# Optimization experiments

Hardware: AMD Instinct MI355X
Metric: run time of the kernel (lower is better)

The kernel has to match this reference:

```python
import jax, jax.numpy as jnp
import numpy as np

B, H, L, N = 8, 512, 2048, 64  # batch, channels (vmapped width), seq len (l_max), state size
DT_MIN, DT_MAX = 0.01, 1.0


def setup_inputs() -> dict:
    key = jax.random.key(0)
    k1, k2, k3 = jax.random.split(key, 3)
    u = jax.random.normal(k1, (B, H, L), dtype=jnp.float32)
    # 'lin' scaling init: A_re = -0.5, A_im = pi * arange(N), per channel
    A_re = -0.5 * jnp.ones((H, N), jnp.float32)
    A_im = jnp.pi * jnp.broadcast_to(jnp.arange(N, dtype=jnp.float32), (H, N))
    C = jax.random.normal(k2, (H, N, 2), jnp.float32) * jnp.float32(0.5 ** 0.5)
    D = jnp.ones((H,), jnp.float32)
    log_step = (jax.random.uniform(k3, (H,), jnp.float32)
                * (jnp.log(DT_MAX) - jnp.log(DT_MIN)) + jnp.log(DT_MIN))
    return dict(u=u, A_re=A_re, A_im=A_im, C=C, D=D, log_step=log_step)


def reference(u, A_re, A_im, C, D, log_step):
    Lq = u.shape[-1]
    # A = clip(A_re, max=-1e-4) + i*A_im  (H, N) complex
    A = jnp.minimum(A_re, -1e-4) + 1j * A_im
    Cc = C[..., 0] + 1j * C[..., 1]                 # (H, N)
    step = jnp.exp(log_step)                        # (H,)
    dtA = step[:, None] * A                         # (H, N)
    # ZOH kernel: K[h,l] = Re( sum_n C[h,n] * (exp(dtA)-1)/A * exp(dtA)^l )
    coef = Cc * (jnp.exp(dtA) - 1.0) / A            # (H, N)
    ells = jnp.arange(Lq, dtype=jnp.float32)
    expmat = jnp.exp(dtA[:, :, None] * ells)        # (H, N, L) complex
    K = jnp.einsum('hn,hnl->hl', coef, expmat).real  # (H, L)
    # FFT causal convolution: pad to 2L (as in the original: pad u by len(K), K by len(u))
    n2 = 2 * Lq
    Ud = jnp.fft.rfft(u, n=n2, axis=-1)             # (B, H, L+1)
    Kd = jnp.fft.rfft(K, n=n2, axis=-1)             # (H, L+1)
    conv = jnp.fft.irfft(Ud * Kd[None], n=n2, axis=-1)[..., :Lq]
    return conv + D[None, :, None] * u
```

## Files before the change

kernel.cpp:

```cpp
#include <hip/hip_runtime.h>
#include <math.h>


typedef short bf16x8 __attribute__((ext_vector_type(8)));
typedef float f32x4  __attribute__((ext_vector_type(4)));

#define NCHK 32
#define USTR 68
#define ESTR 66
#define MFMA __builtin_amdgcn_mfma_f32_16x16x32_bf16

static __device__ __forceinline__ short f2bf(float x){
    unsigned u = __float_as_uint(x);
    u += 0x7FFFu + ((u >> 16) & 1u);
    return (short)(u >> 16);
}
static __device__ __forceinline__ float bf2f(short h){
    return __uint_as_float(((unsigned)(unsigned short)h) << 16);
}
static __device__ __forceinline__ void split8(const float* f, bf16x8& hi, bf16x8& lo){
    #pragma unroll
    for (int i=0;i<8;++i){
        const short hv = f2bf(f[i]);
        hi[i] = hv;
        lo[i] = f2bf(f[i] - bf2f(hv));
    }
}
static __device__ __forceinline__ void cmul(float& xr, float& xi, float yr, float yi){
    const float t = xr*yr - xi*yi;
    xi = xr*yi + xi*yr;
    xr = t;
}

__global__ void __launch_bounds__(256, 3) s4d_mfma4(
    const float* __restrict__ u_g, const float* __restrict__ A_re,
    const float* __restrict__ A_im, const float* __restrict__ Cg,
    const float* __restrict__ Dp, const float* __restrict__ log_step,
    float* __restrict__ out, int B, int H, int L)
{
    const int h    = blockIdx.x;
    const int tid  = threadIdx.x;
    const int wv   = tid >> 6;
    const int lane = tid & 63;
    const int l15  = lane & 15;
    const int oct  = lane >> 4;

    __shared__ __align__(16) float u_s[2][NCHK][USTR];
    __shared__ __align__(16) char  pool2[34816];
    __shared__ float K_s[64];

    float (*w_s)[NCHK][USTR] = (float (*)[NCHK][USTR])pool2;
    float (*S_s)[NCHK][USTR] = (float (*)[NCHK][USTR])(pool2 + 17408);
    float* Ef = (float*)pool2;

    const float dt = expf(log_step[h]);

    const float are = fminf(A_re[h*64 + lane], -1e-4f);
    const float aim = A_im[h*64 + lane];
    const float dre = dt * are, dim = dt * aim;
    float sn_, cs_;
    const float er = expf(dre);
    sincosf(dim, &sn_, &cs_);
    const float rre = er * cs_, rim = er * sn_;
    const float den = are*are + aim*aim;
    const float ir  = are/den, ii = -aim/den;
    const float c0r = Cg[(h*64+lane)*2 + 0];
    const float c0i = Cg[(h*64+lane)*2 + 1];
    const float e1r = rre - 1.0f, e1i = rim;
    const float ttr = e1r*ir - e1i*ii;
    const float tti = e1r*ii + e1i*ir;
    const float cre = c0r*ttr - c0i*tti;
    const float cim = c0r*tti + c0i*ttr;

    {
        const float* up = u_g + (size_t)h * (size_t)L;
        float4 a0 = *(const float4*)(up + tid*8);
        float4 a1 = *(const float4*)(up + tid*8 + 4);
        const int ch = (tid*8) >> 6, t0 = (tid*8) & 63;
        *(float4*)&u_s[0][ch][t0]   = a0;
        *(float4*)&u_s[0][ch][t0+4] = a1;
    }

    float rhor, rhoi;
    {
        float qre = rre, qim = rim;
        #pragma unroll
        for (int i=0;i<4;++i){ const float t2=qre*qre-qim*qim; qim=2.0f*qre*qim; qre=t2; }
        rhor = qre; rhoi = qim;
        cmul(rhor, rhoi, rhor, rhoi);
        cmul(rhor, rhoi, rhor, rhoi);
        float wre = 1.0f, wim = 0.0f;
        for (int i=0;i<wv;++i) cmul(wre, wim, qre, qim);
        float mre = cre*wre - cim*wim;
        float mim = cre*wim + cim*wre;
        #pragma unroll
        for (int jj=0;jj<16;++jj){
            const int p = wv*16 + jj;
            float red = mre;
            #pragma unroll
            for (int off=32; off; off>>=1) red += __shfl_xor(red, off);
            if (lane == 0) K_s[p] = red;
            Ef[p*ESTR + lane]      = mre;
            Ef[(65+p)*ESTR + lane] = -mim;
            cmul(mre, mim, rre, rim);
        }
        if (wv == 3){
            Ef[64*ESTR + lane]      = mre;
            Ef[(65+64)*ESTR + lane] = -mim;
        }
    }
    __syncthreads();

    bf16x8 Whre[2], Wlre[2], Whim[2], Wlim[2];
    bf16x8 Mhre[2], Mlre[2], Mhni[2], Mlni[2];
    bf16x8 Th[2],  Tl[2];
    {
        const int nw = wv*16 + l15;
        const float aw = fminf(A_re[h*64+nw], -1e-4f);
        const float bw = A_im[h*64+nw];
        const float dr = dt*aw, di = dt*bw;
        float s1, c1; const float e1 = expf(dr); sincosf(di, &s1, &c1);
        const float rwr = e1*c1, rwi = e1*s1;
        #pragma unroll
        for (int kh=0; kh<2; ++kh){
            const int elo = 63 - (kh*32 + oct*8) - 7;
            float s2, c2;
            const float e2 = expf(dr*(float)elo); sincosf(di*(float)elo, &s2, &c2);
            float vr = e2*c2, vi = e2*s2;
            float fr[8], fi[8];
            fr[7] = vr; fi[7] = vi;
            #pragma unroll
            for (int i=6;i>=0;--i){
                cmul(vr, vi, rwr, rwi);
                fr[i] = vr; fi[i] = vi;
            }
            split8(fr, Whre[kh], Wlre[kh]);
            split8(fi, Whim[kh], Wlim[kh]);
        }
        const int jp1 = wv*16 + l15 + 1;
        #pragma unroll
        for (int kh=0; kh<2; ++kh){
            const int n0 = kh*32 + oct*8;
            float fm[8];
            #pragma unroll
            for (int i=0;i<8;++i) fm[i] = Ef[jp1*ESTR + n0 + i];
            split8(fm, Mhre[kh], Mlre[kh]);
            #pragma unroll
            for (int i=0;i<8;++i) fm[i] = Ef[(65+jp1)*ESTR + n0 + i];
            split8(fm, Mhni[kh], Mlni[kh]);
            float ft[8];
            #pragma unroll
            for (int i=0;i<8;++i){
                const int d = (wv*16 + l15) - (n0 + i);
                ft[i] = (d > 0) ? K_s[d] : 0.0f;
            }
            split8(ft, Th[kh], Tl[kh]);
        }
    }
    const float DK = Dp[h] + K_s[0];
    __syncthreads();

    for (int b=0; b<B; ++b){
        const int buf = b & 1;
        const size_t obase = ((size_t)b*H + h) * (size_t)L;
        float4 p0 = {0,0,0,0}, p1 = {0,0,0,0};
        const bool pf = (b+1 < B);
        if (pf){
            const float* up = u_g + ((size_t)(b+1)*H + h) * (size_t)L;
            p0 = *(const float4*)(up + tid*8);
            p1 = *(const float4*)(up + tid*8 + 4);
        }
        bf16x8 Uh[2][2], Ul[2][2];
        #pragma unroll
        for (int ct=0; ct<2; ++ct){
            const int ch = ct*16 + l15;
            #pragma unroll
            for (int kh=0; kh<2; ++kh){
                const float4 x0 = *(const float4*)&u_s[buf][ch][kh*32 + oct*8];
                const float4 x1 = *(const float4*)&u_s[buf][ch][kh*32 + oct*8 + 4];
                const float f[8] = {x0.x,x0.y,x0.z,x0.w,x1.x,x1.y,x1.z,x1.w};
                split8(f, Uh[ct][kh], Ul[ct][kh]);
            }
        }
        #pragma unroll
        for (int ct=0; ct<2; ++ct){
            f32x4 ar = {0.f,0.f,0.f,0.f}, ai = {0.f,0.f,0.f,0.f};
            #pragma unroll
            for (int kh=0; kh<2; ++kh){
                ar = MFMA(Whre[kh], Uh[ct][kh], ar, 0,0,0);
                ar = MFMA(Whre[kh], Ul[ct][kh], ar, 0,0,0);
                ar = MFMA(Wlre[kh], Uh[ct][kh], ar, 0,0,0);
                ai = MFMA(Whim[kh], Uh[ct][kh], ai, 0,0,0);
                ai = MFMA(Whim[kh], Ul[ct][kh], ai, 0,0,0);
                ai = MFMA(Wlim[kh], Uh[ct][kh], ai, 0,0,0);
            }
            const int ch = ct*16 + l15;
            const int n0 = wv*16 + oct*4;
            *(f32x4*)&w_s[0][ch][n0] = ar;
            *(f32x4*)&w_s[1][ch][n0] = ai;
        }
        __syncthreads();
        if (wv == 0){
            float sr = 0.0f, si = 0.0f;
            #pragma unroll 4
            for (int k=0;k<NCHK;++k){
                S_s[0][k][lane] = sr; S_s[1][k][lane] = si;
                const float wr = w_s[0][k][lane];
                const float wi = w_s[1][k][lane];
                const float t2 = fmaf(rhor, sr, fmaf(-rhoi, si, wr));
                si = fmaf(rhor, si, fmaf(rhoi, sr, wi));
                sr = t2;
            }
        }
        __syncthreads();
        #pragma unroll
        for (int ct=0; ct<2; ++ct){
            const int ch = ct*16 + l15;
            bf16x8 Srh[2], Srl[2], Sih[2], Sil[2];
            #pragma unroll
            for (int kh=0; kh<2; ++kh){
                {
                    const float4 x0 = *(const float4*)&S_s[0][ch][kh*32+oct*8];
                    const float4 x1 = *(const float4*)&S_s[0][ch][kh*32+oct*8+4];
                    const float f[8] = {x0.x,x0.y,x0.z,x0.w,x1.x,x1.y,x1.z,x1.w};
                    split8(f, Srh[kh], Srl[kh]);
                }
                {
                    const float4 x0 = *(const float4*)&S_s[1][ch][kh*32+oct*8];
                    const float4 x1 = *(const float4*)&S_s[1][ch][kh*32+oct*8+4];
                    const float f[8] = {x0.x,x0.y,x0.z,x0.w,x1.x,x1.y,x1.z,x1.w};
                    split8(f, Sih[kh], Sil[kh]);
                }
            }
            f32x4 acc = {0.f,0.f,0.f,0.f};
            #pragma unroll
            for (int kh=0; kh<2; ++kh){
                acc = MFMA(Mhre[kh], Srh[kh], acc, 0,0,0);
                acc = MFMA(Mhre[kh], Srl[kh], acc, 0,0,0);
                acc = MFMA(Mlre[kh], Srh[kh], acc, 0,0,0);
                acc = MFMA(Mhni[kh], Sih[kh], acc, 0,0,0);
                acc = MFMA(Mhni[kh], Sil[kh], acc, 0,0,0);
                acc = MFMA(Mlni[kh], Sih[kh], acc, 0,0,0);
                acc = MFMA(Th[kh], Uh[ct][kh], acc, 0,0,0);
                acc = MFMA(Th[kh], Ul[ct][kh], acc, 0,0,0);
                acc = MFMA(Tl[kh], Uh[ct][kh], acc, 0,0,0);
            }
            const int j0 = wv*16 + oct*4;
            const float4 uu = *(const float4*)&u_s[buf][ch][j0];
            float4 y;
            y.x = acc[0] + DK*uu.x;
            y.y = acc[1] + DK*uu.y;
            y.z = acc[2] + DK*uu.z;
            y.w = acc[3] + DK*uu.w;
            *(float4*)(out + obase + (size_t)(ch*64 + j0)) = y;
        }
        if (pf){
            const int ch2 = (tid*8) >> 6, t0 = (tid*8) & 63;
            *(float4*)&u_s[buf^1][ch2][t0]   = p0;
            *(float4*)&u_s[buf^1][ch2][t0+4] = p1;
        }
        __syncthreads();
    }
}

extern "C" void kernel_launch(void* const* d_in, const int* in_sizes, int n_in,
                              void* d_out, int out_size, void* d_ws, size_t ws_size,
                              hipStream_t stream) {
    const float* u        = (const float*)d_in[0];
    const float* A_re     = (const float*)d_in[1];
    const float* A_im     = (const float*)d_in[2];
    const float* C        = (const float*)d_in[3];
    const float* Dp       = (const float*)d_in[4];
    const float* log_step = (const float*)d_in[5];
    float* out = (float*)d_out;

    const int H = in_sizes[4];
    const int L = 2048;
    const int B = in_sizes[0] / (H * L);
    (void)d_ws; (void)ws_size; (void)out_size; (void)n_in;

    dim3 grid(H);
    dim3 block(256);
    hipLaunchKernelGGL(s4d_mfma4, grid, block, 0, stream,
                       u, A_re, A_im, C, Dp, log_step, out, B, H, L);
}
```

Baseline: 56.46 us.

## Double block to 512 threads, split chunk tiles across wave pairs, stage output through LDS

Raises the block size from 256 to 512 threads (8 waves). Each wave now handles one 16-channel chunk tile per batch instead of two, which halves the per-wave MFMA work and register footprint. The kernel power rho = r^64 is now computed as (r^8)^8 to match the new 8-wave E-table setup. Outputs are written to LDS and then stored fully coalesced, one float4 per thread, at the cost of an extra __syncthreads per batch. The serial scan still runs on a single wave, so more waves mostly adds latency hiding and more barrier cost.

```diff
diff --git a/kernel.cpp b/kernel.cpp
--- a/kernel.cpp
+++ b/kernel.cpp
@@ -32,7 +32,7 @@
     xr = t;
 }
 
-__global__ void __launch_bounds__(256, 3) s4d_mfma4(
+__global__ void __launch_bounds__(512, 4) s4d_r8(
     const float* __restrict__ u_g, const float* __restrict__ A_re,
     const float* __restrict__ A_im, const float* __restrict__ Cg,
     const float* __restrict__ Dp, const float* __restrict__ log_step,
@@ -41,6 +41,8 @@
     const int h    = blockIdx.x;
     const int tid  = threadIdx.x;
     const int wv   = tid >> 6;
+    const int wr   = wv & 3;
+    const int wc   = wv >> 2;
     const int lane = tid & 63;
     const int l15  = lane & 15;
     const int oct  = lane >> 4;
@@ -74,28 +76,26 @@
 
     {
         const float* up = u_g + (size_t)h * (size_t)L;
-        float4 a0 = *(const float4*)(up + tid*8);
-        float4 a1 = *(const float4*)(up + tid*8 + 4);
-        const int ch = (tid*8) >> 6, t0 = (tid*8) & 63;
-        *(float4*)&u_s[0][ch][t0]   = a0;
-        *(float4*)&u_s[0][ch][t0+4] = a1;
+        const float4 a0 = *(const float4*)(up + tid*4);
+        const int ch = tid >> 4, t0 = (tid & 15) * 4;
+        *(float4*)&u_s[0][ch][t0] = a0;
     }
 
     float rhor, rhoi;
     {
-        float qre = rre, qim = rim;
-        #pragma unroll
-        for (int i=0;i<4;++i){ const float t2=qre*qre-qim*qim; qim=2.0f*qre*qim; qre=t2; }
-        rhor = qre; rhoi = qim;
-        cmul(rhor, rhoi, rhor, rhoi);
-        cmul(rhor, rhoi, rhor, rhoi);
+        float r8r = rre, r8i = rim;
+        #pragma unroll
+        for (int i=0;i<3;++i){ const float t2=r8r*r8r-r8i*r8i; r8i=2.0f*r8r*r8i; r8r=t2; }
+        rhor = r8r; rhoi = r8i;
+        #pragma unroll
+        for (int i=0;i<3;++i){ const float t2=rhor*rhor-rhoi*rhoi; rhoi=2.0f*rhor*rhoi; rhor=t2; }
         float wre = 1.0f, wim = 0.0f;
-        for (int i=0;i<wv;++i) cmul(wre, wim, qre, qim);
+        for (int i=0;i<wv;++i) cmul(wre, wim, r8r, r8i);
         float mre = cre*wre - cim*wim;
         float mim = cre*wim + cim*wre;
         #pragma unroll
-        for (int jj=0;jj<16;++jj){
-            const int p = wv*16 + jj;
+        for (int jj=0;jj<8;++jj){
+            const int p = wv*8 + jj;
             float red = mre;
             #pragma unroll
             for (int off=32; off; off>>=1) red += __shfl_xor(red, off);
@@ -104,7 +104,7 @@
             Ef[(65+p)*ESTR + lane] = -mim;
             cmul(mre, mim, rre, rim);
         }
-        if (wv == 3){
+        if (wv == 7){
             Ef[64*ESTR + lane]      = mre;
             Ef[(65+64)*ESTR + lane] = -mim;
         }
@@ -115,7 +115,7 @@
     bf16x8 Mhre[2], Mlre[2], Mhni[2], Mlni[2];
     bf16x8 Th[2],  Tl[2];
     {
-        const int nw = wv*16 + l15;
+        const int nw = wr*16 + l15;
         const float aw = fminf(A_re[h*64+nw], -1e-4f);
         const float bw = A_im[h*64+nw];
         const float dr = dt*aw, di = dt*bw;
@@ -137,7 +137,7 @@
             split8(fr, Whre[kh], Wlre[kh]);
             split8(fi, Whim[kh], Wlim[kh]);
         }
-        const int jp1 = wv*16 + l15 + 1;
+        const int jp1 = wr*16 + l15 + 1;
         #pragma unroll
         for (int kh=0; kh<2; ++kh){
             const int n0 = kh*32 + oct*8;
@@ -151,7 +151,7 @@
             float ft[8];
             #pragma unroll
             for (int i=0;i<8;++i){
-                const int d = (wv*16 + l15) - (n0 + i);
+                const int d = (wr*16 + l15) - (n0 + i);
                 ft[i] = (d > 0) ? K_s[d] : 0.0f;
             }
             split8(ft, Th[kh], Tl[kh]);
@@ -163,41 +163,35 @@
     for (int b=0; b<B; ++b){
         const int buf = b & 1;
         const size_t obase = ((size_t)b*H + h) * (size_t)L;
-        float4 p0 = {0,0,0,0}, p1 = {0,0,0,0};
+        float4 pf0 = {0,0,0,0};
         const bool pf = (b+1 < B);
         if (pf){
             const float* up = u_g + ((size_t)(b+1)*H + h) * (size_t)L;
-            p0 = *(const float4*)(up + tid*8);
-            p1 = *(const float4*)(up + tid*8 + 4);
-        }
-        bf16x8 Uh[2][2], Ul[2][2];
-        #pragma unroll
-        for (int ct=0; ct<2; ++ct){
-            const int ch = ct*16 + l15;
+            pf0 = *(const float4*)(up + tid*4);
+        }
+        bf16x8 Uh[2], Ul[2];
+        const int chU = wc*16 + l15;
+        #pragma unroll
+        for (int kh=0; kh<2; ++kh){
+            const float4 x0 = *(const float4*)&u_s[buf][chU][kh*32 + oct*8];
+            const float4 x1 = *(const float4*)&u_s[buf][chU][kh*32 + oct*8 + 4];
+            const float f[8] = {x0.x,x0.y,x0.z,x0.w,x1.x,x1.y,x1.z,x1.w};
+            split8(f, Uh[kh], Ul[kh]);
+        }
+        {
+            f32x4 ar = {0.f,0.f,0.f,0.f}, ai = {0.f,0.f,0.f,0.f};
             #pragma unroll
             for (int kh=0; kh<2; ++kh){
-                const float4 x0 = *(const float4*)&u_s[buf][ch][kh*32 + oct*8];
-                const float4 x1 = *(const float4*)&u_s[buf][ch][kh*32 + oct*8 + 4];
-                const float f[8] = {x0.x,x0.y,x0.z,x0.w,x1.x,x1.y,x1.z,x1.w};
-                split8(f, Uh[ct][kh], Ul[ct][kh]);
-            }
-        }
-        #pragma unroll
-        for (int ct=0; ct<2; ++ct){
-            f32x4 ar = {0.f,0.f,0.f,0.f}, ai = {0.f,0.f,0.f,0.f};
-            #pragma unroll
-            for (int kh=0; kh<2; ++kh){
-                ar = MFMA(Whre[kh], Uh[ct][kh], ar, 0,0,0);
-                ar = MFMA(Whre[kh], Ul[ct][kh], ar, 0,0,0);
-                ar = MFMA(Wlre[kh], Uh[ct][kh], ar, 0,0,0);
-                ai = MFMA(Whim[kh], Uh[ct][kh], ai, 0,0,0);
-                ai = MFMA(Whim[kh], Ul[ct][kh], ai, 0,0,0);
-                ai = MFMA(Wlim[kh], Uh[ct][kh], ai, 0,0,0);
-            }
-            const int ch = ct*16 + l15;
-            const int n0 = wv*16 + oct*4;
-            *(f32x4*)&w_s[0][ch][n0] = ar;
-            *(f32x4*)&w_s[1][ch][n0] = ai;
+                ar = MFMA(Whre[kh], Uh[kh], ar, 0,0,0);
+                ar = MFMA(Whre[kh], Ul[kh], ar, 0,0,0);
+                ar = MFMA(Wlre[kh], Uh[kh], ar, 0,0,0);
+                ai = MFMA(Whim[kh], Uh[kh], ai, 0,0,0);
+                ai = MFMA(Whim[kh], Ul[kh], ai, 0,0,0);
+                ai = MFMA(Wlim[kh], Uh[kh], ai, 0,0,0);
+            }
+            const int n0 = wr*16 + oct*4;
+            *(f32x4*)&w_s[0][chU][n0] = ar;
+            *(f32x4*)&w_s[1][chU][n0] = ai;
         }
         __syncthreads();
         if (wv == 0){
@@ -205,29 +199,27 @@
             #pragma unroll 4
             for (int k=0;k<NCHK;++k){
                 S_s[0][k][lane] = sr; S_s[1][k][lane] = si;
-                const float wr = w_s[0][k][lane];
-                const float wi = w_s[1][k][lane];
-                const float t2 = fmaf(rhor, sr, fmaf(-rhoi, si, wr));
-                si = fmaf(rhor, si, fmaf(rhoi, sr, wi));
+                const float wr2 = w_s[0][k][lane];
+                const float wi2 = w_s[1][k][lane];
+                const float t2 = fmaf(rhor, sr, fmaf(-rhoi, si, wr2));
+                si = fmaf(rhor, si, fmaf(rhoi, sr, wi2));
                 sr = t2;
             }
         }
         __syncthreads();
-        #pragma unroll
-        for (int ct=0; ct<2; ++ct){
-            const int ch = ct*16 + l15;
+        {
             bf16x8 Srh[2], Srl[2], Sih[2], Sil[2];
             #pragma unroll
             for (int kh=0; kh<2; ++kh){
                 {
-                    const float4 x0 = *(const float4*)&S_s[0][ch][kh*32+oct*8];
-                    const float4 x1 = *(const float4*)&S_s[0][ch][kh*32+oct*8+4];
+                    const float4 x0 = *(const float4*)&S_s[0][chU][kh*32+oct*8];
+                    const float4 x1 = *(const float4*)&S_s[0][chU][kh*32+oct*8+4];
                     const float f[8] = {x0.x,x0.y,x0.z,x0.w,x1.x,x1.y,x1.z,x1.w};
                     split8(f, Srh[kh], Srl[kh]);
                 }
                 {
-                    const float4 x0 = *(const float4*)&S_s[1][ch][kh*32+oct*8];
-                    const float4 x1 = *(const float4*)&S_s[1][ch][kh*32+oct*8+4];
+                    const float4 x0 = *(const float4*)&S_s[1][chU][kh*32+oct*8];
+                    const float4 x1 = *(const float4*)&S_s[1][chU][kh*32+oct*8+4];
                     const float f[8] = {x0.x,x0.y,x0.z,x0.w,x1.x,x1.y,x1.z,x1.w};
                     split8(f, Sih[kh], Sil[kh]);
                 }
@@ -241,23 +233,28 @@
                 acc = MFMA(Mhni[kh], Sih[kh], acc, 0,0,0);
                 acc = MFMA(Mhni[kh], Sil[kh], acc, 0,0,0);
                 acc = MFMA(Mlni[kh], Sih[kh], acc, 0,0,0);
-                acc = MFMA(Th[kh], Uh[ct][kh], acc, 0,0,0);
-                acc = MFMA(Th[kh], Ul[ct][kh], acc, 0,0,0);
-                acc = MFMA(Tl[kh], Uh[ct][kh], acc, 0,0,0);
-            }
-            const int j0 = wv*16 + oct*4;
-            const float4 uu = *(const float4*)&u_s[buf][ch][j0];
+                acc = MFMA(Th[kh], Uh[kh], acc, 0,0,0);
+                acc = MFMA(Th[kh], Ul[kh], acc, 0,0,0);
+                acc = MFMA(Tl[kh], Uh[kh], acc, 0,0,0);
+            }
+            const int j0 = wr*16 + oct*4;
+            *(f32x4*)&w_s[0][chU][j0] = acc;
+        }
+        __syncthreads();
+        {
+            const int ch = tid >> 4, t0 = (tid & 15) * 4;
+            const float4 yv = *(const float4*)&w_s[0][ch][t0];
+            const float4 uu = *(const float4*)&u_s[buf][ch][t0];
             float4 y;
-            y.x = acc[0] + DK*uu.x;
-            y.y = acc[1] + DK*uu.y;
-            y.z = acc[2] + DK*uu.z;
-            y.w = acc[3] + DK*uu.w;
-            *(float4*)(out + obase + (size_t)(ch*64 + j0)) = y;
+            y.x = yv.x + DK*uu.x;
+            y.y = yv.y + DK*uu.y;
+            y.z = yv.z + DK*uu.z;
+            y.w = yv.w + DK*uu.w;
+            *(float4*)(out + obase + (size_t)(tid*4)) = y;
         }
         if (pf){
-            const int ch2 = (tid*8) >> 6, t0 = (tid*8) & 63;
-            *(float4*)&u_s[buf^1][ch2][t0]   = p0;
-            *(float4*)&u_s[buf^1][ch2][t0+4] = p1;
+            const int ch = tid >> 4, t0 = (tid & 15) * 4;
+            *(float4*)&u_s[buf^1][ch][t0] = pf0;
         }
         __syncthreads();
     }
@@ -280,7 +277,7 @@
     (void)d_ws; (void)ws_size; (void)out_size; (void)n_in;
 
     dim3 grid(H);
-    dim3 block(256);
-    hipLaunchKernelGGL(s4d_mfma4, grid, block, 0, stream,
+    dim3 block(512);
+    hipLaunchKernelGGL(s4d_r8, grid, block, 0, stream,
                        u, A_re, A_im, C, Dp, log_step, out, B, H, L);
 }
```

Result: slower. 76.56 us (+35.6%).
